# Kernel tuning notes

Measured on AMD Instinct MI355X. Metric: run time of the kernel, lower is better.

The kernel has to match this reference:

```python
import jax, jax.numpy as jnp
import numpy as np

ORDER = 2
BN_EPS = 1e-5

def setup_inputs() -> dict:
    key = jax.random.key(0)
    ks = jax.random.split(key, 8)
    B, N, L, H = 32, 512, 12, 64
    S = 2                      # support_len
    OUT = 64                   # out_dim
    M = ORDER * S * H          # einsum middle dim = 256
    x = jax.random.normal(ks[0], (B, N, L, H), dtype=jnp.float32)
    # row-scaled random diffusion matrices to keep multi-hop propagation stable
    support = jax.random.uniform(ks[1], (S, N, N), dtype=jnp.float32) / N
    scale = 1.0 / M
    weight = scale * jax.random.normal(ks[2], (L, M, OUT), dtype=jnp.float32)
    eps = jnp.zeros((1,), dtype=jnp.float32)
    gamma = jnp.ones((OUT,), dtype=jnp.float32)
    beta = jnp.zeros((OUT,), dtype=jnp.float32)
    w2 = jax.random.normal(ks[3], (OUT, OUT), dtype=jnp.float32) / np.sqrt(OUT)
    b2 = jnp.zeros((OUT,), dtype=jnp.float32)
    return {"x": x, "support": support, "weight": weight, "eps": eps,
            "gamma": gamma, "beta": beta, "w2": w2, "b2": b2}

def reference(x, support, weight, eps, gamma, beta, w2, b2):
    B, N, L, H = x.shape
    xv = x.reshape(B, N, L * H)            # [B,N,LH]
    res = []
    for i in range(support.shape[0]):      # small fixed loop over supports
        A = support[i]                     # [N,N]
        out = xv
        for _ in range(ORDER):
            out = (1.0 + eps) * out + jnp.einsum('nm,bmd->bnd', A, out)
            res.append(out)
    out = jnp.stack(res, axis=-1)          # [B,N,LH,K], K = order*support_len
    K = out.shape[-1]
    out = out.reshape(B, N, L, H * K)      # [B,N,L,M]
    out = jnp.einsum('bnlm,lmo->bno', out, weight)   # [B,N,OUT]
    # dropout is identity in eval mode
    C = out.shape[-1]
    flat = out.reshape(B * N, C)
    mean = flat.mean(axis=0)
    var = flat.var(axis=0)                 # biased, matching torch BN training
    normed = (flat - mean) * jax.lax.rsqrt(var + BN_EPS) * gamma + beta
    y = jax.nn.relu(normed.reshape(B, N, C))
    return jnp.einsum('bnc,oc->bno', y, w2) + b2
```

## Files before the change

kernel.cpp:

```cpp
#include <hip/hip_runtime.h>
#include <hip/hip_bf16.h>
#include <cstddef>
#include <cstdint>

#define B_   32
#define N_   512
#define D_   768
#define OUT_ 64
#define R_   (B_ * N_)

typedef unsigned short u16;
typedef __bf16 bf16x8 __attribute__((ext_vector_type(8)));
typedef float  f32x4  __attribute__((ext_vector_type(4)));
typedef unsigned short u16x8 __attribute__((ext_vector_type(8)));

__device__ __forceinline__ u16 f2bf(float f) {
    __hip_bfloat16 h = __float2bfloat16(f);
    return __builtin_bit_cast(u16, h);
}

__device__ __forceinline__ f32x4 mfma16(u16x8 a, u16x8 b, f32x4 c) {
    return __builtin_amdgcn_mfma_f32_16x16x32_bf16(
        __builtin_bit_cast(bf16x8, a), __builtin_bit_cast(bf16x8, b), c, 0, 0, 0);
}

__device__ __forceinline__ void gl2lds16(const void* g, void* l) {
    __builtin_amdgcn_global_load_lds(
        (const __attribute__((address_space(1))) unsigned int*)g,
        (__attribute__((address_space(3))) unsigned int*)l, 16, 0, 0);
}

__global__ __launch_bounds__(256) void prep2(
    const float* __restrict__ support, const float* __restrict__ weight,
    const float* __restrict__ epsp,
    u16* __restrict__ MallC, u16* __restrict__ MT, u16* __restrict__ Wt)
{
    const int blk = blockIdx.x, tid = threadIdx.x;
    __shared__ float t[32][33];
    if (blk < 512) {
        int s = blk >> 8, rem = blk & 255;
        int n0 = (rem >> 4) * 32, m0 = (rem & 15) * 32;
        const float f = 1.0f + epsp[0];
        const float* S = support + (size_t)s * 262144;
#pragma unroll
        for (int p = 0; p < 4; ++p) {
            int nl = p * 8 + (tid >> 5), ml = tid & 31;
            float v = S[(size_t)(n0 + nl) * 512 + m0 + ml];
            if (n0 + nl == m0 + ml) v += f;
            MallC[(size_t)(n0 + nl) * 2048 + s * 1024 + m0 + ml] = f2bf(v);
            t[nl][ml] = v;
        }
        __syncthreads();
#pragma unroll
        for (int p = 0; p < 4; ++p) {
            int ml = p * 8 + (tid >> 5), nl = tid & 31;
            MT[(size_t)s * 262144 + (size_t)(m0 + ml) * 512 + n0 + nl] = f2bf(t[nl][ml]);
        }
    } else {
        int idx = (blk - 512) * 256 + tid;
        int k = idx / 49152, rem = idx % 49152;
        int o = rem / 768, d = rem % 768;
        int l = d >> 6, hh = d & 63;
        Wt[idx] = f2bf(weight[((size_t)l * 256 + hh * 4 + k) * 64 + o]);
    }
}

__global__ __launch_bounds__(256, 2) void zmsq(
    const u16* __restrict__ Wt, const float* __restrict__ x,
    const u16* __restrict__ MallC_in, const u16* __restrict__ MT,
    u16* __restrict__ Z, u16* __restrict__ MallC_out)
{
    __shared__ __align__(16) u16 SM[40960];
    const int tid = threadIdx.x, lane = tid & 63, wid = tid >> 6;
    const int lrow = lane & 15, lk8 = (lane >> 4) * 8;
    const int q = lane >> 4;
    const int bid = blockIdx.x;

    if (bid < 256) {
        const int b = bid >> 3, m0 = (bid & 7) * 64;
        u16* Abuf = SM;
        u16* Bbuf = SM + 32768;

        const u16* gsrcA[8]; u16* ldstA[8];
#pragma unroll
        for (int t = 0; t < 8; ++t) {
            int idx = wid * 8 + t;
            int p = idx >> 4, g = idx & 15;
            gsrcA[t] = Wt + (size_t)(g * 16 + lrow) * 768 + p * 32 + lk8;
            ldstA[t] = Abuf + p * 8192 + g * 512;
        }
        const int r = tid >> 2, c4 = tid & 3;
        const float* gx = x + (size_t)(b * 512 + m0 + r) * 768 + c4 * 16;
        u16* bdst = Bbuf + (c4 >> 1) * 2048 + (r >> 4) * 512
                  + (c4 & 1) * 256 + (r & 15) * 8;

        f32x4 acc[4][4] = {};

        {
            f32x4 a0 = *(const f32x4*)(gx);
            f32x4 a1 = *(const f32x4*)(gx + 4);
            f32x4 a2 = *(const f32x4*)(gx + 8);
            f32x4 a3 = *(const f32x4*)(gx + 12);
#pragma unroll
            for (int t = 0; t < 8; ++t) gl2lds16(gsrcA[t], ldstA[t]);
            u16x8 w0, w1;
#pragma unroll
            for (int j = 0; j < 4; ++j) {
                w0[j] = f2bf(a0[j]); w0[4 + j] = f2bf(a1[j]);
                w1[j] = f2bf(a2[j]); w1[4 + j] = f2bf(a3[j]);
            }
            *(u16x8*)(bdst)       = w0;
            *(u16x8*)(bdst + 128) = w1;
        }

#pragma unroll 2
        for (int kk = 0; kk < 12; ++kk) {
            const int cbA = (kk & 1) * 16384, nbA = cbA ^ 16384;
            const int cbB = (kk & 1) * 4096,  nbB = cbB ^ 4096;
            __syncthreads();
            f32x4 a0, a1, a2, a3;
            if (kk < 11) {
                const float* g = gx + (kk + 1) * 64;
                a0 = *(const f32x4*)(g);
                a1 = *(const f32x4*)(g + 4);
                a2 = *(const f32x4*)(g + 8);
                a3 = *(const f32x4*)(g + 12);
#pragma unroll
                for (int t = 0; t < 8; ++t)
                    gl2lds16(gsrcA[t] + (kk + 1) * 64, ldstA[t] + nbA);
            }
#pragma unroll
            for (int p = 0; p < 2; ++p) {
                u16x8 af[4], bq[4];
#pragma unroll
                for (int f = 0; f < 4; ++f)
                    af[f] = *(const u16x8*)(Abuf + cbA + p * 8192 + (wid * 4 + f) * 512 + lane * 8);
#pragma unroll
                for (int f = 0; f < 4; ++f)
                    bq[f] = *(const u16x8*)(Bbuf + cbB + p * 2048 + f * 512 + lane * 8);
#pragma unroll
                for (int fi = 0; fi < 4; ++fi)
#pragma unroll
                    for (int fj = 0; fj < 4; ++fj)
                        acc[fi][fj] = mfma16(af[fi], bq[fj], acc[fi][fj]);
            }
            if (kk < 11) {
                u16x8 w0, w1;
#pragma unroll
                for (int j = 0; j < 4; ++j) {
                    w0[j] = f2bf(a0[j]); w0[4 + j] = f2bf(a1[j]);
                    w1[j] = f2bf(a2[j]); w1[4 + j] = f2bf(a3[j]);
                }
                *(u16x8*)(bdst + nbB)       = w0;
                *(u16x8*)(bdst + nbB + 128) = w1;
            }
        }
        __syncthreads();

        u16* scr = SM;
#pragma unroll
        for (int fi = 0; fi < 4; ++fi)
#pragma unroll
            for (int fj = 0; fj < 4; ++fj)
#pragma unroll
                for (int rr = 0; rr < 4; ++rr)
                    scr[(wid * 64 + fi * 16 + q * 4 + rr) * 72 + fj * 16 + lrow]
                        = f2bf(acc[fi][fj][rr]);
        __syncthreads();
        const int c8 = (tid & 7) * 8, rg = tid >> 3;
#pragma unroll
        for (int i = 0; i < 8; ++i) {
            int srow = i * 32 + rg;
            u16x8 v = *(const u16x8*)(scr + srow * 72 + c8);
            int o = srow & 63, k = srow >> 6;
            *(u16x8*)(Z + (size_t)(b * 64 + o) * 2048 + k * 512 + m0 + c8) = v;
        }
    } else {
        const int lb = bid - 256;
        const int s = lb >> 6, i0 = ((lb >> 3) & 7) * 64, j0 = (lb & 7) * 64;
        const int wr = wid >> 1, wc = wid & 1;

        const u16* gsrc[4]; u16* ldst[4];
#pragma unroll
        for (int t = 0; t < 4; ++t) {
            int idx = wid * 4 + t;
            if (idx < 8) {
                int p = idx >> 2, sub = idx & 3;
                gsrc[t] = MallC_in + (size_t)(i0 + sub * 16 + lrow) * 2048 + s * 1024 + p * 32 + lk8;
                ldst[t] = SM + p * 2048 + sub * 512;
            } else {
                int i2 = idx - 8;
                int p = i2 >> 2, sub = i2 & 3;
                gsrc[t] = MT + (size_t)s * 262144 + (size_t)(j0 + sub * 16 + lrow) * 512 + p * 32 + lk8;
                ldst[t] = SM + 4096 + p * 2048 + sub * 512;
            }
        }
        f32x4 acc[2][2] = {};
#pragma unroll
        for (int t = 0; t < 4; ++t) gl2lds16(gsrc[t], ldst[t]);
#pragma unroll 2
        for (int kk = 0; kk < 8; ++kk) {
            const int cb = (kk & 1) * 8192, nb = cb ^ 8192;
            __syncthreads();
            if (kk < 7) {
#pragma unroll
                for (int t = 0; t < 4; ++t)
                    gl2lds16(gsrc[t] + (kk + 1) * 64, ldst[t] + nb);
            }
#pragma unroll
            for (int p = 0; p < 2; ++p) {
                u16x8 af[2], bq[2];
#pragma unroll
                for (int f = 0; f < 2; ++f)
                    af[f] = *(const u16x8*)(SM + cb + p * 2048 + (wr * 2 + f) * 512 + lane * 8);
#pragma unroll
                for (int f = 0; f < 2; ++f)
                    bq[f] = *(const u16x8*)(SM + cb + 4096 + p * 2048 + (wc * 2 + f) * 512 + lane * 8);
#pragma unroll
                for (int fi = 0; fi < 2; ++fi)
#pragma unroll
                    for (int fj = 0; fj < 2; ++fj)
                        acc[fi][fj] = mfma16(af[fi], bq[fj], acc[fi][fj]);
            }
        }
#pragma unroll
        for (int fi = 0; fi < 2; ++fi)
#pragma unroll
            for (int fj = 0; fj < 2; ++fj)
#pragma unroll
                for (int rr = 0; rr < 4; ++rr) {
                    int n = i0 + wr * 32 + fi * 16 + q * 4 + rr;
                    int c = j0 + wc * 32 + fj * 16 + lrow;
                    MallC_out[(size_t)n * 2048 + (2 * s + 1) * 512 + c] = f2bf(acc[fi][fj][rr]);
                }
    }
}

__global__ __launch_bounds__(256, 4) void ysum(
    const u16* __restrict__ G, const u16* __restrict__ Z, float* __restrict__ Yh)
{
    __shared__ __align__(16) u16 SM[16384];
    const int tid = threadIdx.x, lane = tid & 63, wid = tid >> 6;
    const int wr = wid >> 1, wc = wid & 1;
    const int lrow = lane & 15, lk8 = (lane >> 4) * 8;
    const int bid = blockIdx.x;
    const int kq = bid >> 8, rt = bid & 255;
    const int r0 = rt * 64, b = rt >> 3, n0 = r0 & 511;

    const u16* gsrc[4]; u16* ldst[4];
#pragma unroll
    for (int t = 0; t < 4; ++t) {
        int idx = wid * 4 + t;
        if (idx < 8) {
            int p = idx >> 2, sub = idx & 3;
            gsrc[t] = G + (size_t)(n0 + sub * 16 + lrow) * 2048 + kq * 512 + p * 32 + lk8;
            ldst[t] = SM + p * 2048 + sub * 512;
        } else {
            int i2 = idx - 8;
            int p = i2 >> 2, sub = i2 & 3;
            gsrc[t] = Z + (size_t)(b * 64 + sub * 16 + lrow) * 2048 + kq * 512 + p * 32 + lk8;
            ldst[t] = SM + 4096 + p * 2048 + sub * 512;
        }
    }
    f32x4 acc[2][2] = {};
#pragma unroll
    for (int t = 0; t < 4; ++t) gl2lds16(gsrc[t], ldst[t]);
#pragma unroll 2
    for (int kk = 0; kk < 8; ++kk) {
        const int cb = (kk & 1) * 8192, nb = cb ^ 8192;
        __syncthreads();
        if (kk < 7) {
#pragma unroll
            for (int t = 0; t < 4; ++t)
                gl2lds16(gsrc[t] + (kk + 1) * 64, ldst[t] + nb);
        }
#pragma unroll
        for (int p = 0; p < 2; ++p) {
            u16x8 af[2], bq[2];
#pragma unroll
            for (int f = 0; f < 2; ++f)
                af[f] = *(const u16x8*)(SM + cb + p * 2048 + (wr * 2 + f) * 512 + lane * 8);
#pragma unroll
            for (int f = 0; f < 2; ++f)
                bq[f] = *(const u16x8*)(SM + cb + 4096 + p * 2048 + (wc * 2 + f) * 512 + lane * 8);
#pragma unroll
            for (int fi = 0; fi < 2; ++fi)
#pragma unroll
                for (int fj = 0; fj < 2; ++fj)
                    acc[fi][fj] = mfma16(af[fi], bq[fj], acc[fi][fj]);
        }
    }
    const int q = lane >> 4;
    float* Yk = Yh + (size_t)kq * R_ * 64;
#pragma unroll
    for (int fi = 0; fi < 2; ++fi)
#pragma unroll
        for (int fj = 0; fj < 2; ++fj)
#pragma unroll
            for (int rr = 0; rr < 4; ++rr) {
                int r2 = r0 + wr * 32 + fi * 16 + q * 4 + rr;
                int o  = wc * 32 + fj * 16 + lrow;
                Yk[(size_t)r2 * 64 + o] = acc[fi][fj][rr];
            }
}

__global__ __launch_bounds__(256) void bn_part(
    const float* __restrict__ Yh, float* __restrict__ part, float* __restrict__ Y)
{
    const int blk = blockIdx.x, tid = threadIdx.x;
    const int o = tid & 63, g = tid >> 6;
    float s = 0.f, s2 = 0.f;
#pragma unroll
    for (int p = 0; p < 16; ++p) {
        int r = blk * 64 + p * 4 + g;
        size_t off = (size_t)r * 64 + o;
        float v = Yh[off] + Yh[(size_t)R_ * 64 + off]
                + Yh[(size_t)2 * R_ * 64 + off] + Yh[(size_t)3 * R_ * 64 + off];
        Y[off] = v;
        s += v; s2 += v * v;
    }
    __shared__ float ls[4][64], ls2[4][64];
    ls[g][o] = s; ls2[g][o] = s2;
    __syncthreads();
    if (tid < 64) {
        float t = 0.f, t2 = 0.f;
#pragma unroll
        for (int g2 = 0; g2 < 4; ++g2) { t += ls[g2][tid]; t2 += ls2[g2][tid]; }
        part[blk * 128 + tid]      = t;
        part[blk * 128 + 64 + tid] = t2;
    }
}

__global__ __launch_bounds__(256) void bn_out(
    const float* __restrict__ Y, const float* __restrict__ part,
    const float* __restrict__ gamma, const float* __restrict__ beta,
    const float* __restrict__ w2, const float* __restrict__ b2,
    float* __restrict__ out)
{
    __shared__ float ys[64 * 68];
    __shared__ float w2s[64 * 65];
    __shared__ float red[4][64], red2[4][64];
    __shared__ float sa[64], sh[64];
    const int tid = threadIdx.x;
    const int r0 = blockIdx.x * 64;
    const int o = tid & 63, g = tid >> 6;
    {
        float s = 0.f, s2 = 0.f;
        for (int p = g; p < 256; p += 4) {
            s  += part[p * 128 + o];
            s2 += part[p * 128 + 64 + o];
        }
        red[g][o] = s; red2[g][o] = s2;
    }
#pragma unroll
    for (int i = 0; i < 16; ++i) {
        int idx = tid + i * 256;
        w2s[(idx >> 6) * 65 + (idx & 63)] = w2[idx];
    }
    __syncthreads();
    if (tid < 64) {
        float t0 = red[0][tid] + red[1][tid] + red[2][tid] + red[3][tid];
        float t2 = red2[0][tid] + red2[1][tid] + red2[2][tid] + red2[3][tid];
        float mean = t0 * (1.0f / R_);
        float var  = t2 * (1.0f / R_) - mean * mean;
        float a = rsqrtf(var + 1e-5f) * gamma[tid];
        sa[tid] = a;
        sh[tid] = beta[tid] - mean * a;
    }
    __syncthreads();
    {
        float a = sa[o], bsh = sh[o];
#pragma unroll
        for (int p = 0; p < 16; ++p) {
            int rl = p * 4 + g;
            size_t off = (size_t)(r0 + rl) * 64 + o;
            float v = Y[off];
            ys[o * 68 + rl] = fmaxf(fmaf(v, a, bsh), 0.f);
        }
    }
    __syncthreads();
    float acc[16];
    float bb = b2[o];
#pragma unroll
    for (int j = 0; j < 16; ++j) acc[j] = bb;
    for (int c = 0; c < 64; ++c) {
        float wv = w2s[o * 65 + c];
        const float* yr = ys + c * 68 + g * 16;
        f32x4 y0 = *(const f32x4*)(yr);
        f32x4 y1 = *(const f32x4*)(yr + 4);
        f32x4 y2 = *(const f32x4*)(yr + 8);
        f32x4 y3 = *(const f32x4*)(yr + 12);
#pragma unroll
        for (int j = 0; j < 4; ++j) {
            acc[j]      = fmaf(wv, y0[j], acc[j]);
            acc[4 + j]  = fmaf(wv, y1[j], acc[4 + j]);
            acc[8 + j]  = fmaf(wv, y2[j], acc[8 + j]);
            acc[12 + j] = fmaf(wv, y3[j], acc[12 + j]);
        }
    }
#pragma unroll
    for (int j = 0; j < 16; ++j)
        out[(size_t)(r0 + g * 16 + j) * OUT_ + o] = acc[j];
}

extern "C" void kernel_launch(void* const* d_in, const int* in_sizes, int n_in,
                              void* d_out, int out_size, void* d_ws, size_t ws_size,
                              hipStream_t stream)
{
    const float* x       = (const float*)d_in[0];
    const float* support = (const float*)d_in[1];
    const float* weight  = (const float*)d_in[2];
    const float* eps     = (const float*)d_in[3];
    const float* gamma   = (const float*)d_in[4];
    const float* beta    = (const float*)d_in[5];
    const float* w2      = (const float*)d_in[6];
    const float* b2      = (const float*)d_in[7];
    float* out = (float*)d_out;

    char* ws = (char*)d_ws;
    u16*   MallC = (u16*)(ws);
    u16*   MT    = (u16*)(ws + 2097152);
    u16*   Wt    = (u16*)(ws + 3145728);
    u16*   Z     = (u16*)(ws + 3538944);
    float* Yh    = (float*)(ws + 11927552);
    float* part  = (float*)(ws + 28704768);
    float* Y     = (float*)(ws + 28835840);

    prep2  <<<1280, 256, 0, stream>>>(support, weight, eps, MallC, MT, Wt);
    zmsq   <<<384,  256, 0, stream>>>(Wt, x, MallC, MT, Z, MallC);
    ysum   <<<1024, 256, 0, stream>>>(MallC, Z, Yh);
    bn_part<<<256,  256, 0, stream>>>(Yh, part, Y);
    bn_out <<<256,  256, 0, stream>>>(Y, part, gamma, beta, w2, b2, out);
}
```

Measured before the change: 163.4 us.

## Fuse ysum split-K GEMM with BN partial statistics into one kernel

Drops the 4-way split-K of the ysum GEMM, so each 512-thread block accumulates the full K=2048 reduction for a 64x64 output tile. The block then computes the BatchNorm partial sums and sums of squares from the tile staged in LDS. This removes the Yh partial-sum buffer and the separate bn_part launch, along with the write and re-read of four fp32 partial outputs. In exchange the grid shrinks from 1024 to 256 blocks, each with a longer serial K loop and a larger LDS footprint, which may reduce parallelism and occupancy.

Result: no change. 160.9 us (-1.5%).

```diff
diff --git a/kernel.cpp b/kernel.cpp
--- a/kernel.cpp
+++ b/kernel.cpp
@@ -236,98 +236,83 @@
     }
 }
 
-__global__ __launch_bounds__(256, 4) void ysum(
-    const u16* __restrict__ G, const u16* __restrict__ Z, float* __restrict__ Yh)
+__global__ __launch_bounds__(512) void ysumY(
+    const u16* __restrict__ G, const u16* __restrict__ Z,
+    float* __restrict__ Y, float* __restrict__ part)
 {
-    __shared__ __align__(16) u16 SM[16384];
+    __shared__ __align__(16) u16 SM[32768];
     const int tid = threadIdx.x, lane = tid & 63, wid = tid >> 6;
-    const int wr = wid >> 1, wc = wid & 1;
+    const int wr = wid >> 2, wc = wid & 3;
     const int lrow = lane & 15, lk8 = (lane >> 4) * 8;
-    const int bid = blockIdx.x;
-    const int kq = bid >> 8, rt = bid & 255;
-    const int r0 = rt * 64, b = rt >> 3, n0 = r0 & 511;
+    const int rt = blockIdx.x;
+    const int r0 = rt * 64, b = rt >> 3, n0 = (rt & 7) * 64;
 
     const u16* gsrc[4]; u16* ldst[4];
 #pragma unroll
     for (int t = 0; t < 4; ++t) {
         int idx = wid * 4 + t;
-        if (idx < 8) {
+        if (idx < 16) {
             int p = idx >> 2, sub = idx & 3;
-            gsrc[t] = G + (size_t)(n0 + sub * 16 + lrow) * 2048 + kq * 512 + p * 32 + lk8;
+            gsrc[t] = G + (size_t)(n0 + sub * 16 + lrow) * 2048 + p * 32 + lk8;
             ldst[t] = SM + p * 2048 + sub * 512;
         } else {
-            int i2 = idx - 8;
+            int i2 = idx - 16;
             int p = i2 >> 2, sub = i2 & 3;
-            gsrc[t] = Z + (size_t)(b * 64 + sub * 16 + lrow) * 2048 + kq * 512 + p * 32 + lk8;
-            ldst[t] = SM + 4096 + p * 2048 + sub * 512;
-        }
-    }
-    f32x4 acc[2][2] = {};
+            gsrc[t] = Z + (size_t)(b * 64 + sub * 16 + lrow) * 2048 + p * 32 + lk8;
+            ldst[t] = SM + 8192 + p * 2048 + sub * 512;
+        }
+    }
+    f32x4 acc[2] = {};
 #pragma unroll
     for (int t = 0; t < 4; ++t) gl2lds16(gsrc[t], ldst[t]);
 #pragma unroll 2
-    for (int kk = 0; kk < 8; ++kk) {
-        const int cb = (kk & 1) * 8192, nb = cb ^ 8192;
+    for (int kk = 0; kk < 16; ++kk) {
+        const int cb = (kk & 1) * 16384, nb = cb ^ 16384;
         __syncthreads();
-        if (kk < 7) {
+        if (kk < 15) {
 #pragma unroll
             for (int t = 0; t < 4; ++t)
-                gl2lds16(gsrc[t] + (kk + 1) * 64, ldst[t] + nb);
-        }
-#pragma unroll
-        for (int p = 0; p < 2; ++p) {
-            u16x8 af[2], bq[2];
-#pragma unroll
-            for (int f = 0; f < 2; ++f)
-                af[f] = *(const u16x8*)(SM + cb + p * 2048 + (wr * 2 + f) * 512 + lane * 8);
-#pragma unroll
-            for (int f = 0; f < 2; ++f)
-                bq[f] = *(const u16x8*)(SM + cb + 4096 + p * 2048 + (wc * 2 + f) * 512 + lane * 8);
-#pragma unroll
-            for (int fi = 0; fi < 2; ++fi)
-#pragma unroll
-                for (int fj = 0; fj < 2; ++fj)
-                    acc[fi][fj] = mfma16(af[fi], bq[fj], acc[fi][fj]);
-        }
-    }
+                gl2lds16(gsrc[t] + (kk + 1) * 128, ldst[t] + nb);
+        }
+#pragma unroll
+        for (int p = 0; p < 4; ++p) {
+            u16x8 bq = *(const u16x8*)(SM + cb + 8192 + p * 2048 + wc * 512 + lane * 8);
+#pragma unroll
+            for (int f = 0; f < 2; ++f) {
+                u16x8 af = *(const u16x8*)(SM + cb + p * 2048 + (wr * 2 + f) * 512 + lane * 8);
+                acc[f] = mfma16(af, bq, acc[f]);
+            }
+        }
+    }
+    __syncthreads();
+
+    float* ls = (float*)SM;
     const int q = lane >> 4;
-    float* Yk = Yh + (size_t)kq * R_ * 64;
-#pragma unroll
-    for (int fi = 0; fi < 2; ++fi)
-#pragma unroll
-        for (int fj = 0; fj < 2; ++fj)
-#pragma unroll
-            for (int rr = 0; rr < 4; ++rr) {
-                int r2 = r0 + wr * 32 + fi * 16 + q * 4 + rr;
-                int o  = wc * 32 + fj * 16 + lrow;
-                Yk[(size_t)r2 * 64 + o] = acc[fi][fj][rr];
-            }
-}
-
-__global__ __launch_bounds__(256) void bn_part(
-    const float* __restrict__ Yh, float* __restrict__ part, float* __restrict__ Y)
-{
-    const int blk = blockIdx.x, tid = threadIdx.x;
+#pragma unroll
+    for (int f = 0; f < 2; ++f)
+#pragma unroll
+        for (int rr = 0; rr < 4; ++rr)
+            ls[(wr * 32 + f * 16 + q * 4 + rr) * 68 + wc * 16 + lrow] = acc[f][rr];
+    __syncthreads();
     const int o = tid & 63, g = tid >> 6;
     float s = 0.f, s2 = 0.f;
 #pragma unroll
-    for (int p = 0; p < 16; ++p) {
-        int r = blk * 64 + p * 4 + g;
-        size_t off = (size_t)r * 64 + o;
-        float v = Yh[off] + Yh[(size_t)R_ * 64 + off]
-                + Yh[(size_t)2 * R_ * 64 + off] + Yh[(size_t)3 * R_ * 64 + off];
-        Y[off] = v;
+    for (int pp = 0; pp < 8; ++pp) {
+        int rr2 = pp * 8 + g;
+        float v = ls[rr2 * 68 + o];
+        Y[(size_t)(r0 + rr2) * 64 + o] = v;
         s += v; s2 += v * v;
     }
-    __shared__ float ls[4][64], ls2[4][64];
-    ls[g][o] = s; ls2[g][o] = s2;
+    float* rs  = (float*)(SM + 16384);
+    float* rs2 = rs + 512;
+    rs[g * 64 + o] = s; rs2[g * 64 + o] = s2;
     __syncthreads();
     if (tid < 64) {
-        float t = 0.f, t2 = 0.f;
-#pragma unroll
-        for (int g2 = 0; g2 < 4; ++g2) { t += ls[g2][tid]; t2 += ls2[g2][tid]; }
-        part[blk * 128 + tid]      = t;
-        part[blk * 128 + 64 + tid] = t2;
+        float t1 = 0.f, t2 = 0.f;
+#pragma unroll
+        for (int gg = 0; gg < 8; ++gg) { t1 += rs[gg * 64 + tid]; t2 += rs2[gg * 64 + tid]; }
+        part[rt * 128 + tid]      = t1;
+        part[rt * 128 + 64 + tid] = t2;
     }
 }
 
@@ -422,13 +407,11 @@
     u16*   MT    = (u16*)(ws + 2097152);
     u16*   Wt    = (u16*)(ws + 3145728);
     u16*   Z     = (u16*)(ws + 3538944);
-    float* Yh    = (float*)(ws + 11927552);
     float* part  = (float*)(ws + 28704768);
     float* Y     = (float*)(ws + 28835840);
 
     prep2  <<<1280, 256, 0, stream>>>(support, weight, eps, MallC, MT, Wt);
     zmsq   <<<384,  256, 0, stream>>>(Wt, x, MallC, MT, Z, MallC);
-    ysum   <<<1024, 256, 0, stream>>>(MallC, Z, Yh);
-    bn_part<<<256,  256, 0, stream>>>(Yh, part, Y);
+    ysumY  <<<256,  512, 0, stream>>>(MallC, Z, Y, part);
     bn_out <<<256,  256, 0, stream>>>(Y, part, gamma, beta, w2, b2, out);
 }
```
